# Kernel optimization log

Hardware: AMD Instinct MI355X
Metric: run time of the kernel (lower is better)

Reference implementation:

```python
import jax, jax.numpy as jnp
import numpy as np

FEATURE_DIM = 1024
NUM_TASKS = 8
BATCH = 4096


def setup_inputs() -> dict:
    key = jax.random.key(0)
    k1, k2, k3, k4, k5 = jax.random.split(key, 5)
    features = jax.random.normal(k1, (BATCH, FEATURE_DIM), dtype=jnp.float32)
    eps = jax.random.normal(k2, (NUM_TASKS,), dtype=jnp.float32)
    # variational params: mean ~ N(0, 0.01), logvar = -3.0 (per __init__)
    mean = 0.01 * jax.random.normal(k3, (NUM_TASKS,), dtype=jnp.float32)
    logvar = jnp.full((NUM_TASKS,), -3.0, dtype=jnp.float32)
    # task matrices: randn * 0.01
    task_mats = 0.01 * jax.random.normal(k4, (NUM_TASKS, FEATURE_DIM, FEATURE_DIM), dtype=jnp.float32)
    # projection initialized to identity (nn.init.eye_)
    proj_w = jnp.eye(FEATURE_DIM, dtype=jnp.float32)
    return {"features": features, "eps": eps, "mean": mean,
            "logvar": logvar, "task_mats": task_mats, "proj_w": proj_w}


def reference(features, eps, mean, logvar, task_mats, proj_w):
    # coefficients via reparameterization trick (logvar clamped to [-8, 2])
    lv = jnp.clip(logvar, -8.0, 2.0)
    coeff = mean + eps * jnp.exp(0.5 * lv)  # [T]

    # sequential task-vector composition, batched over all rows at once:
    #   x <- x + c_j * (x @ M_j)  for j = 0..T-1
    def step(x, cm):
        c, M = cm
        x = x + c * (x @ M)  # [B, D]
        return x, None

    x, _ = jax.lax.scan(step, features, (coeff, task_mats))
    # nn.Linear(bias=False): y = x @ W^T
    out = x @ proj_w.T  # [B, D]
    return out
```

## Files before the change

### kernel.cpp

```cpp
#include <hip/hip_runtime.h>
#include <stdint.h>

#define FEAT 1024
#define BATCH 4096
#define SM (FEAT * FEAT)

typedef float f32x4 __attribute__((ext_vector_type(4)));
typedef short bf16x8 __attribute__((ext_vector_type(8)));
typedef unsigned short u16x8 __attribute__((ext_vector_type(8)));
typedef unsigned short u16x4 __attribute__((ext_vector_type(4)));

__device__ inline unsigned short f32_to_bf16(float f) {
  union { float f; uint32_t u; } v; v.f = f;
  uint32_t u = v.u;
  uint32_t lsb = (u >> 16) & 1u;
  u += 0x7fffu + lsb;
  return (unsigned short)(u >> 16);
}

__device__ inline float bf16_to_f32(unsigned short h) {
  union { uint32_t u; float f; } v; v.u = (uint32_t)h << 16; return v.f;
}

__device__ inline void gload_lds16(const void* g, void* l) {
  __builtin_amdgcn_global_load_lds(
      (__attribute__((address_space(1))) void*)(g),
      (__attribute__((address_space(3))) void*)(l),
      16, 0, 0);
}

__global__ void conv_all(const float* __restrict__ M, const float* __restrict__ feat,
                         const float* __restrict__ pw, const float* __restrict__ mean,
                         const float* __restrict__ eps, const float* __restrict__ logvar,
                         unsigned short* __restrict__ Dr, unsigned short* __restrict__ Dt,
                         unsigned short* __restrict__ Xb, unsigned short* __restrict__ Wb) {
  const int bid = blockIdx.x;
  const int t = threadIdx.x;
  if (bid < 2048) {
    __shared__ unsigned short Ts[64][68];
    const int j = bid >> 8, rem = bid & 255;
    const int n0 = (rem >> 4) * 64, k0 = (rem & 15) * 64;
    float lv = fminf(fmaxf(logvar[j], -8.f), 2.f);
    const float c = mean[j] + eps[j] * expf(0.5f * lv);
    const float* src = M + (size_t)j * SM;
    unsigned short* dr = Dr + (size_t)j * SM;
#pragma unroll
    for (int i2 = 0; i2 < 4; ++i2) {
      int fidx = i2 * 256 + t;
      int kl = fidx >> 4, nf = fidx & 15;
      float4 v = *(const float4*)(src + (size_t)(k0 + kl) * FEAT + n0 + nf * 4);
      u16x4 o;
      o[0] = f32_to_bf16(c * v.x); o[1] = f32_to_bf16(c * v.y);
      o[2] = f32_to_bf16(c * v.z); o[3] = f32_to_bf16(c * v.w);
      *(u16x4*)&Ts[kl][nf * 4] = o;
      *(u16x4*)(dr + (size_t)(k0 + kl) * FEAT + n0 + nf * 4) = o;
    }
    __syncthreads();
    if (j & 1) {
      unsigned short* dt = Dt + (size_t)(j >> 1) * SM;
#pragma unroll
      for (int i2 = 0; i2 < 2; ++i2) {
        int cidx = t * 2 + i2;
        int nl = cidx >> 3, kc = (cidx & 7) * 8;
        u16x8 o;
#pragma unroll
        for (int r = 0; r < 8; ++r) o[r] = Ts[kc + r][nl];
        *(u16x8*)(dt + (size_t)(n0 + nl) * FEAT + k0 + kc) = o;
      }
    }
  } else {
    for (int i = (bid - 2048) * 256 + t; i < 655360; i += 65536) {
      const float* in; unsigned short* o8; int ci;
      if (i < 524288) { in = feat; o8 = Xb; ci = i; }
      else            { in = pw;   o8 = Wb; ci = i - 524288; }
      const float4* p = (const float4*)in + (size_t)ci * 2;
      float4 a = p[0], b = p[1];
      u16x8 o;
      o[0] = f32_to_bf16(a.x); o[1] = f32_to_bf16(a.y);
      o[2] = f32_to_bf16(a.z); o[3] = f32_to_bf16(a.w);
      o[4] = f32_to_bf16(b.x); o[5] = f32_to_bf16(b.y);
      o[6] = f32_to_bf16(b.z); o[7] = f32_to_bf16(b.w);
      *((u16x8*)o8 + ci) = o;
    }
  }
}

#define WAIT_VM(n)                                            \
  do {                                                        \
    if ((n) == 0) asm volatile("s_waitcnt vmcnt(0)" ::: "memory");   \
    else if ((n) == 1) asm volatile("s_waitcnt vmcnt(%0)" :: "i"(NT) : "memory"); \
    else asm volatile("s_waitcnt vmcnt(%0)" :: "i"(2 * NT) : "memory"); \
  } while (0)

__device__ __forceinline__ void gemm_core128(
    const unsigned short* __restrict__ Ap, const unsigned short* __restrict__ Btp,
    int arow0, int bcol0, int t,
    unsigned short* As, unsigned short* Bs, f32x4 (&acc)[4][2]) {
  constexpr int NT = 6;
  const int lane = t & 63;
  const int wid = t >> 6, wm = wid >> 1, wn = wid & 1;
  const int ar = t >> 3;
  const int acb = (((t & 7) ^ ((t >> 3) & 7)) << 4);
  const unsigned short* Abase = Ap + (size_t)(arow0 + ar) * FEAT + (acb >> 1);
  const unsigned short* Bbase = Btp + (size_t)(bcol0 + ar) * FEAT + (acb >> 1);
  unsigned short* AsP = As + t * 8;
  unsigned short* BsP = Bs + t * 8;

#pragma unroll
  for (int kt = 0; kt < 2; ++kt) {
    const int ko = kt * 64;
#pragma unroll
    for (int p = 0; p < 4; ++p)
      gload_lds16(Abase + (size_t)(p * 32) * FEAT + ko, AsP + kt * 8192 + p * 2048);
#pragma unroll
    for (int p = 0; p < 2; ++p)
      gload_lds16(Bbase + (size_t)(p * 32) * FEAT + ko, BsP + kt * 4096 + p * 2048);
  }

  int o0 = 0, o1 = 1, o2 = 2;
#pragma unroll
  for (int kt = 0; kt < 16; ++kt) {
    if (kt + 2 < 16) {
      const int ko = (kt + 2) * 64;
#pragma unroll
      for (int p = 0; p < 4; ++p)
        gload_lds16(Abase + (size_t)(p * 32) * FEAT + ko, AsP + o2 * 8192 + p * 2048);
#pragma unroll
      for (int p = 0; p < 2; ++p)
        gload_lds16(Bbase + (size_t)(p * 32) * FEAT + ko, BsP + o2 * 4096 + p * 2048);
      WAIT_VM(2);
    } else if (kt + 1 < 16) {
      WAIT_VM(1);
    } else {
      WAIT_VM(0);
    }
    __builtin_amdgcn_s_barrier();
    __builtin_amdgcn_sched_barrier(0);
    const char* Asc = (const char*)(As + o0 * 8192);
    const char* Bsc = (const char*)(Bs + o0 * 4096);
#pragma unroll
    for (int kk = 0; kk < 2; ++kk) {
      bf16x8 a[4], b[2];
      const int cbase = kk * 64 + ((lane >> 4) << 4);
#pragma unroll
      for (int m = 0; m < 4; ++m) {
        int r = wm * 64 + m * 16 + (lane & 15);
        a[m] = *(const bf16x8*)(Asc + r * 128 + (cbase ^ ((r & 7) << 4)));
      }
#pragma unroll
      for (int n = 0; n < 2; ++n) {
        int r = wn * 32 + n * 16 + (lane & 15);
        b[n] = *(const bf16x8*)(Bsc + r * 128 + (cbase ^ ((r & 7) << 4)));
      }
#pragma unroll
      for (int m = 0; m < 4; ++m)
#pragma unroll
        for (int n = 0; n < 2; ++n)
          acc[m][n] = __builtin_amdgcn_mfma_f32_16x16x32_bf16(a[m], b[n], acc[m][n], 0, 0, 0);
    }
    __builtin_amdgcn_s_barrier();
    __builtin_amdgcn_sched_barrier(0);
    const int tmp = o0; o0 = o1; o1 = o2; o2 = tmp;
  }
}

template <int MODE>
__global__ __launch_bounds__(256, 2) void gemm128(
    const unsigned short* __restrict__ A, const unsigned short* __restrict__ Bt,
    const unsigned short* __restrict__ lin,
    unsigned short* __restrict__ O1, unsigned short* __restrict__ O2,
    float* __restrict__ outf) {
  __shared__ __align__(16) unsigned short ldsbuf[36864];
  unsigned short* As = ldsbuf;
  unsigned short* Bs = ldsbuf + 24576;

  const int t = threadIdx.x;
  const int lane = t & 63, wid = t >> 6, wm = wid >> 1, wn = wid & 1;
  const int swz = (blockIdx.x & 7) * 64 + (blockIdx.x >> 3);

  int bm, bn, z = 0;
  const unsigned short *Ap, *Btp;
  if (MODE == 0) {
    z = swz >> 7;
    const int rem = swz & 127;
    bm = rem >> 4; bn = rem & 15;
    Ap = A + (size_t)(2 * z) * SM;
    Btp = Bt + (size_t)z * SM;
  } else {
    bm = swz >> 4; bn = swz & 15;
    Ap = A; Btp = Bt;
  }

  f32x4 acc[4][2];
#pragma unroll
  for (int m = 0; m < 4; ++m)
#pragma unroll
    for (int n = 0; n < 2; ++n) acc[m][n] = (f32x4)0.f;

  gemm_core128(Ap, Btp, bm * 128, bn * 64, t, As, Bs, acc);

#pragma unroll
  for (int m = 0; m < 4; ++m) {
    int Rb = bm * 128 + wm * 64 + m * 16 + ((lane >> 4) << 2);
#pragma unroll
    for (int n = 0; n < 2; ++n) {
      int C = bn * 64 + wn * 32 + n * 16 + (lane & 15);
      if (MODE == 0) {
        const unsigned short* aA = lin + (size_t)(2 * z) * SM;
        const unsigned short* aB = lin + (size_t)(2 * z + 1) * SM;
        unsigned short* pr = O1 + (size_t)z * SM;
        u16x4 tp;
#pragma unroll
        for (int r2 = 0; r2 < 4; ++r2) {
          size_t idx = (size_t)(Rb + r2) * FEAT + C;
          float v = acc[m][n][r2] + bf16_to_f32(aA[idx]) + bf16_to_f32(aB[idx]);
          unsigned short h = f32_to_bf16(v);
          pr[idx] = h; tp[r2] = h;
        }
        if (z & 1)
          *(u16x4*)(O2 + (size_t)(z >> 1) * SM + (size_t)C * FEAT + Rb) = tp;
      } else {
#pragma unroll
        for (int r2 = 0; r2 < 4; ++r2)
          outf[(size_t)(Rb + r2) * FEAT + C] = acc[m][n][r2];
      }
    }
  }
}

template <int MODE>
__global__ __launch_bounds__(256, 2) void gemm64(
    const unsigned short* __restrict__ A, const unsigned short* __restrict__ Bt,
    const unsigned short* __restrict__ lin, unsigned short* __restrict__ O) {
  constexpr int NT = 4;
  __shared__ __align__(16) unsigned short ldsbuf[24576];
  unsigned short* As = ldsbuf;
  unsigned short* Bs = ldsbuf + 12288;

  const int t = threadIdx.x;
  const int lane = t & 63, wid = t >> 6, wm = wid >> 1, wn = wid & 1;
  const int nb = (int)gridDim.x;
  const int swz = (blockIdx.x & 7) * (nb >> 3) + (blockIdx.x >> 3);

  int bm, bn, z = 0;
  const unsigned short *Ap, *Btp;
  if (MODE == 0) {
    z = swz >> 8;
    const int tile = swz & 255;
    bm = tile >> 4; bn = tile & 15;
    Ap = A + (size_t)(2 * z) * SM;
    Btp = Bt + (size_t)z * SM;
  } else {
    bm = swz >> 4; bn = swz & 15;
    Ap = A; Btp = Bt;
  }
  const int arow0 = bm * 64, bcol0 = bn * 64;

  f32x4 acc[2][2];
#pragma unroll
  for (int m = 0; m < 2; ++m)
#pragma unroll
    for (int n = 0; n < 2; ++n) acc[m][n] = (f32x4)0.f;

  const int ar = t >> 3;
  const int acb = (((t & 7) ^ ((t >> 3) & 7)) << 4);
  const unsigned short* Abase = Ap + (size_t)(arow0 + ar) * FEAT + (acb >> 1);
  const unsigned short* Bbase = Btp + (size_t)(bcol0 + ar) * FEAT + (acb >> 1);
  unsigned short* AsP = As + t * 8;
  unsigned short* BsP = Bs + t * 8;

#pragma unroll
  for (int kt = 0; kt < 2; ++kt) {
    const int ko = kt * 64;
#pragma unroll
    for (int p = 0; p < 2; ++p)
      gload_lds16(Abase + (size_t)(p * 32) * FEAT + ko, AsP + kt * 4096 + p * 2048);
#pragma unroll
    for (int p = 0; p < 2; ++p)
      gload_lds16(Bbase + (size_t)(p * 32) * FEAT + ko, BsP + kt * 4096 + p * 2048);
  }

  int o0 = 0, o1 = 1, o2 = 2;
#pragma unroll
  for (int kt = 0; kt < 16; ++kt) {
    if (kt + 2 < 16) {
      const int ko = (kt + 2) * 64;
#pragma unroll
      for (int p = 0; p < 2; ++p)
        gload_lds16(Abase + (size_t)(p * 32) * FEAT + ko, AsP + o2 * 4096 + p * 2048);
#pragma unroll
      for (int p = 0; p < 2; ++p)
        gload_lds16(Bbase + (size_t)(p * 32) * FEAT + ko, BsP + o2 * 4096 + p * 2048);
      WAIT_VM(2);
    } else if (kt + 1 < 16) {
      WAIT_VM(1);
    } else {
      WAIT_VM(0);
    }
    __builtin_amdgcn_s_barrier();
    __builtin_amdgcn_sched_barrier(0);
    const char* Asc = (const char*)(As + o0 * 4096);
    const char* Bsc = (const char*)(Bs + o0 * 4096);
#pragma unroll
    for (int kk = 0; kk < 2; ++kk) {
      bf16x8 a[2], b[2];
      const int cbase = kk * 64 + ((lane >> 4) << 4);
#pragma unroll
      for (int m = 0; m < 2; ++m) {
        int r = wm * 32 + m * 16 + (lane & 15);
        a[m] = *(const bf16x8*)(Asc + r * 128 + (cbase ^ ((r & 7) << 4)));
      }
#pragma unroll
      for (int n = 0; n < 2; ++n) {
        int r = wn * 32 + n * 16 + (lane & 15);
        b[n] = *(const bf16x8*)(Bsc + r * 128 + (cbase ^ ((r & 7) << 4)));
      }
#pragma unroll
      for (int m = 0; m < 2; ++m)
#pragma unroll
        for (int n = 0; n < 2; ++n)
          acc[m][n] = __builtin_amdgcn_mfma_f32_16x16x32_bf16(a[m], b[n], acc[m][n], 0, 0, 0);
    }
    __builtin_amdgcn_s_barrier();
    __builtin_amdgcn_sched_barrier(0);
    const int tmp = o0; o0 = o1; o1 = o2; o2 = tmp;
  }

#pragma unroll
  for (int m = 0; m < 2; ++m) {
    int Rb = arow0 + wm * 32 + m * 16 + ((lane >> 4) << 2);
#pragma unroll
    for (int n = 0; n < 2; ++n) {
      int C = bcol0 + wn * 32 + n * 16 + (lane & 15);
      if (MODE == 0) {
        const unsigned short* aA = lin + (size_t)(2 * z) * SM;
        const unsigned short* aB = lin + (size_t)(2 * z + 1) * SM;
        unsigned short* po = O + (size_t)z * SM;
#pragma unroll
        for (int r2 = 0; r2 < 4; ++r2) {
          size_t idx = (size_t)(Rb + r2) * FEAT + C;
          float v = acc[m][n][r2] + bf16_to_f32(aA[idx]) + bf16_to_f32(aB[idx]);
          po[idx] = f32_to_bf16(v);
        }
      } else {
        u16x4 lv = *(const u16x4*)(lin + (size_t)C * FEAT + Rb);
        u16x4 o;
#pragma unroll
        for (int r2 = 0; r2 < 4; ++r2)
          o[r2] = f32_to_bf16(acc[m][n][r2] + bf16_to_f32(lv[r2]));
        *(u16x4*)(O + (size_t)C * FEAT + Rb) = o;
      }
    }
  }
}

extern "C" void kernel_launch(void* const* d_in, const int* in_sizes, int n_in,
                              void* d_out, int out_size, void* d_ws, size_t ws_size,
                              hipStream_t stream) {
  const float* features = (const float*)d_in[0];
  const float* eps      = (const float*)d_in[1];
  const float* mean     = (const float*)d_in[2];
  const float* logvar   = (const float*)d_in[3];
  const float* task_mats= (const float*)d_in[4];
  const float* proj_w   = (const float*)d_in[5];
  float* out = (float*)d_out;

  uint8_t* ws = (uint8_t*)d_ws;
  unsigned short* Dr  = (unsigned short*)(ws);
  unsigned short* Dt  = (unsigned short*)(ws + ((size_t)16 << 20));
  unsigned short* Xb  = (unsigned short*)(ws + ((size_t)24 << 20));
  unsigned short* Wb  = (unsigned short*)(ws + ((size_t)32 << 20));
  unsigned short* P1r = (unsigned short*)(ws + ((size_t)34 << 20));
  unsigned short* P1t = (unsigned short*)(ws + ((size_t)42 << 20));
  unsigned short* P2r = (unsigned short*)(ws + ((size_t)46 << 20));
  unsigned short* Ut  = (unsigned short*)(ws + ((size_t)50 << 20));
  unsigned short* St  = (unsigned short*)(ws + ((size_t)52 << 20));

  conv_all<<<2304, 256, 0, stream>>>(task_mats, features, proj_w, mean, eps, logvar,
                                     Dr, Dt, Xb, Wb);
  gemm128<0><<<512, 256, 0, stream>>>(Dr, Dt, Dr, P1r, P1t, nullptr);
  gemm64<0><<<512, 256, 0, stream>>>(P1r, P1t, P1r, P2r);
  gemm64<1><<<256, 256, 0, stream>>>(P2r + SM, Wb, Wb, Ut);
  gemm64<1><<<256, 256, 0, stream>>>(P2r, Ut, Ut, St);
  gemm128<1><<<512, 256, 0, stream>>>(Xb, St, nullptr, nullptr, nullptr, out);
}
```

Before: 70.15 us.

## Fuse two dependent GEMMs into one launch with per-column counters

Two dependent GEMM launches (U = P2b*W + W, then S = P2a*U + U) are merged into one 512-block kernel. Second-half blocks spin on a per-column atomic counter until the 16 producer blocks for that column finish, which removes one launch gap and lets the two phases overlap. conv_all gets more blocks for the feature/weight conversion and also zeroes the counters. The spin-wait depends on producer blocks being scheduled before consumers, which risks deadlock if the dispatch order changes.

```diff
diff --git a/kernel.cpp b/kernel.cpp
--- a/kernel.cpp
+++ b/kernel.cpp
@@ -33,7 +33,8 @@
                          const float* __restrict__ pw, const float* __restrict__ mean,
                          const float* __restrict__ eps, const float* __restrict__ logvar,
                          unsigned short* __restrict__ Dr, unsigned short* __restrict__ Dt,
-                         unsigned short* __restrict__ Xb, unsigned short* __restrict__ Wb) {
+                         unsigned short* __restrict__ Xb, unsigned short* __restrict__ Wb,
+                         int* __restrict__ cnt) {
   const int bid = blockIdx.x;
   const int t = threadIdx.x;
   if (bid < 2048) {
@@ -69,7 +70,8 @@
       }
     }
   } else {
-    for (int i = (bid - 2048) * 256 + t; i < 655360; i += 65536) {
+    if (bid == 2048 && t < 16) cnt[t] = 0;
+    for (int i = (bid - 2048) * 256 + t; i < 655360; i += 262144) {
       const float* in; unsigned short* o8; int ci;
       if (i < 524288) { in = feat; o8 = Xb; ci = i; }
       else            { in = pw;   o8 = Wb; ci = i - 524288; }
@@ -228,7 +230,6 @@
   }
 }
 
-template <int MODE>
 __global__ __launch_bounds__(256, 2) void gemm64(
     const unsigned short* __restrict__ A, const unsigned short* __restrict__ Bt,
     const unsigned short* __restrict__ lin, unsigned short* __restrict__ O) {
@@ -239,21 +240,13 @@
 
   const int t = threadIdx.x;
   const int lane = t & 63, wid = t >> 6, wm = wid >> 1, wn = wid & 1;
-  const int nb = (int)gridDim.x;
-  const int swz = (blockIdx.x & 7) * (nb >> 3) + (blockIdx.x >> 3);
-
-  int bm, bn, z = 0;
-  const unsigned short *Ap, *Btp;
-  if (MODE == 0) {
-    z = swz >> 8;
-    const int tile = swz & 255;
-    bm = tile >> 4; bn = tile & 15;
-    Ap = A + (size_t)(2 * z) * SM;
-    Btp = Bt + (size_t)z * SM;
-  } else {
-    bm = swz >> 4; bn = swz & 15;
-    Ap = A; Btp = Bt;
-  }
+  const int swz = (blockIdx.x & 7) * 64 + (blockIdx.x >> 3);
+
+  const int z = swz >> 8;
+  const int tile = swz & 255;
+  const int bm = tile >> 4, bn = tile & 15;
+  const unsigned short* Ap = A + (size_t)(2 * z) * SM;
+  const unsigned short* Btp = Bt + (size_t)z * SM;
   const int arow0 = bm * 64, bcol0 = bn * 64;
 
   f32x4 acc[2][2];
@@ -332,25 +325,137 @@
 #pragma unroll
     for (int n = 0; n < 2; ++n) {
       int C = bcol0 + wn * 32 + n * 16 + (lane & 15);
-      if (MODE == 0) {
-        const unsigned short* aA = lin + (size_t)(2 * z) * SM;
-        const unsigned short* aB = lin + (size_t)(2 * z + 1) * SM;
-        unsigned short* po = O + (size_t)z * SM;
-#pragma unroll
-        for (int r2 = 0; r2 < 4; ++r2) {
-          size_t idx = (size_t)(Rb + r2) * FEAT + C;
-          float v = acc[m][n][r2] + bf16_to_f32(aA[idx]) + bf16_to_f32(aB[idx]);
-          po[idx] = f32_to_bf16(v);
-        }
-      } else {
-        u16x4 lv = *(const u16x4*)(lin + (size_t)C * FEAT + Rb);
-        u16x4 o;
-#pragma unroll
-        for (int r2 = 0; r2 < 4; ++r2)
-          o[r2] = f32_to_bf16(acc[m][n][r2] + bf16_to_f32(lv[r2]));
-        *(u16x4*)(O + (size_t)C * FEAT + Rb) = o;
-      }
-    }
+      const unsigned short* aA = lin + (size_t)(2 * z) * SM;
+      const unsigned short* aB = lin + (size_t)(2 * z + 1) * SM;
+      unsigned short* po = O + (size_t)z * SM;
+#pragma unroll
+      for (int r2 = 0; r2 < 4; ++r2) {
+        size_t idx = (size_t)(Rb + r2) * FEAT + C;
+        float v = acc[m][n][r2] + bf16_to_f32(aA[idx]) + bf16_to_f32(aB[idx]);
+        po[idx] = f32_to_bf16(v);
+      }
+    }
+  }
+}
+
+__global__ __launch_bounds__(256, 2) void gemm_us(
+    const unsigned short* __restrict__ P2r, const unsigned short* __restrict__ Wb,
+    unsigned short* __restrict__ Ut, unsigned short* __restrict__ St,
+    int* __restrict__ cnt) {
+  constexpr int NT = 4;
+  __shared__ __align__(16) unsigned short ldsbuf[24576];
+  unsigned short* As = ldsbuf;
+  unsigned short* Bs = ldsbuf + 12288;
+
+  const int bid = (int)blockIdx.x;
+  const int t = threadIdx.x;
+  const int lane = t & 63, wid = t >> 6, wm = wid >> 1, wn = wid & 1;
+  const int half = (bid >> 3) & 1;
+  const int widx = ((bid >> 4) << 3) | (bid & 7);
+  const int bm = widx >> 4, bn = widx & 15;
+  const int arow0 = bm * 64, bcol0 = bn * 64;
+
+  const unsigned short *Ap, *Btp, *lin;
+  unsigned short* O;
+  if (half == 0) { Ap = P2r + SM; Btp = Wb; lin = Wb; O = Ut; }
+  else           { Ap = P2r;      Btp = Ut; lin = Ut; O = St; }
+
+  if (half == 1) {
+    if (t == 0)
+      while (atomicAdd(&cnt[bn], 0) < 16) __builtin_amdgcn_s_sleep(8);
+    __syncthreads();
+    __threadfence();
+  }
+
+  f32x4 acc[2][2];
+#pragma unroll
+  for (int m = 0; m < 2; ++m)
+#pragma unroll
+    for (int n = 0; n < 2; ++n) acc[m][n] = (f32x4)0.f;
+
+  const int ar = t >> 3;
+  const int acb = (((t & 7) ^ ((t >> 3) & 7)) << 4);
+  const unsigned short* Abase = Ap + (size_t)(arow0 + ar) * FEAT + (acb >> 1);
+  const unsigned short* Bbase = Btp + (size_t)(bcol0 + ar) * FEAT + (acb >> 1);
+  unsigned short* AsP = As + t * 8;
+  unsigned short* BsP = Bs + t * 8;
+
+#pragma unroll
+  for (int kt = 0; kt < 2; ++kt) {
+    const int ko = kt * 64;
+#pragma unroll
+    for (int p = 0; p < 2; ++p)
+      gload_lds16(Abase + (size_t)(p * 32) * FEAT + ko, AsP + kt * 4096 + p * 2048);
+#pragma unroll
+    for (int p = 0; p < 2; ++p)
+      gload_lds16(Bbase + (size_t)(p * 32) * FEAT + ko, BsP + kt * 4096 + p * 2048);
+  }
+
+  int o0 = 0, o1 = 1, o2 = 2;
+#pragma unroll
+  for (int kt = 0; kt < 16; ++kt) {
+    if (kt + 2 < 16) {
+      const int ko = (kt + 2) * 64;
+#pragma unroll
+      for (int p = 0; p < 2; ++p)
+        gload_lds16(Abase + (size_t)(p * 32) * FEAT + ko, AsP + o2 * 4096 + p * 2048);
+#pragma unroll
+      for (int p = 0; p < 2; ++p)
+        gload_lds16(Bbase + (size_t)(p * 32) * FEAT + ko, BsP + o2 * 4096 + p * 2048);
+      WAIT_VM(2);
+    } else if (kt + 1 < 16) {
+      WAIT_VM(1);
+    } else {
+      WAIT_VM(0);
+    }
+    __builtin_amdgcn_s_barrier();
+    __builtin_amdgcn_sched_barrier(0);
+    const char* Asc = (const char*)(As + o0 * 4096);
+    const char* Bsc = (const char*)(Bs + o0 * 4096);
+#pragma unroll
+    for (int kk = 0; kk < 2; ++kk) {
+      bf16x8 a[2], b[2];
+      const int cbase = kk * 64 + ((lane >> 4) << 4);
+#pragma unroll
+      for (int m = 0; m < 2; ++m) {
+        int r = wm * 32 + m * 16 + (lane & 15);
+        a[m] = *(const bf16x8*)(Asc + r * 128 + (cbase ^ ((r & 7) << 4)));
+      }
+#pragma unroll
+      for (int n = 0; n < 2; ++n) {
+        int r = wn * 32 + n * 16 + (lane & 15);
+        b[n] = *(const bf16x8*)(Bsc + r * 128 + (cbase ^ ((r & 7) << 4)));
+      }
+#pragma unroll
+      for (int m = 0; m < 2; ++m)
+#pragma unroll
+        for (int n = 0; n < 2; ++n)
+          acc[m][n] = __builtin_amdgcn_mfma_f32_16x16x32_bf16(a[m], b[n], acc[m][n], 0, 0, 0);
+    }
+    __builtin_amdgcn_s_barrier();
+    __builtin_amdgcn_sched_barrier(0);
+    const int tmp = o0; o0 = o1; o1 = o2; o2 = tmp;
+  }
+
+#pragma unroll
+  for (int m = 0; m < 2; ++m) {
+    int Rb = arow0 + wm * 32 + m * 16 + ((lane >> 4) << 2);
+#pragma unroll
+    for (int n = 0; n < 2; ++n) {
+      int C = bcol0 + wn * 32 + n * 16 + (lane & 15);
+      u16x4 lv = *(const u16x4*)(lin + (size_t)C * FEAT + Rb);
+      u16x4 o;
+#pragma unroll
+      for (int r2 = 0; r2 < 4; ++r2)
+        o[r2] = f32_to_bf16(acc[m][n][r2] + bf16_to_f32(lv[r2]));
+      *(u16x4*)(O + (size_t)C * FEAT + Rb) = o;
+    }
+  }
+
+  if (half == 0) {
+    __threadfence();
+    __syncthreads();
+    if (t == 0) atomicAdd(&cnt[bn], 1);
   }
 }
 
@@ -375,12 +480,12 @@
   unsigned short* P2r = (unsigned short*)(ws + ((size_t)46 << 20));
   unsigned short* Ut  = (unsigned short*)(ws + ((size_t)50 << 20));
   unsigned short* St  = (unsigned short*)(ws + ((size_t)52 << 20));
-
-  conv_all<<<2304, 256, 0, stream>>>(task_mats, features, proj_w, mean, eps, logvar,
-                                     Dr, Dt, Xb, Wb);
+  int*            cnt = (int*)(ws + ((size_t)54 << 20));
+
+  conv_all<<<3072, 256, 0, stream>>>(task_mats, features, proj_w, mean, eps, logvar,
+                                     Dr, Dt, Xb, Wb, cnt);
   gemm128<0><<<512, 256, 0, stream>>>(Dr, Dt, Dr, P1r, P1t, nullptr);
-  gemm64<0><<<512, 256, 0, stream>>>(P1r, P1t, P1r, P2r);
-  gemm64<1><<<256, 256, 0, stream>>>(P2r + SM, Wb, Wb, Ut);
-  gemm64<1><<<256, 256, 0, stream>>>(P2r, Ut, Ut, St);
+  gemm64<<<512, 256, 0, stream>>>(P1r, P1t, P1r, P2r);
+  gemm_us<<<512, 256, 0, stream>>>(P2r, Wb, Ut, St, cnt);
   gemm128<1><<<512, 256, 0, stream>>>(Xb, St, nullptr, nullptr, nullptr, out);
 }
```

Measured after the change: 129.9 us. +85.2%, slower.
